# Kernel tuning notes

Hardware: AMD Instinct MI355X
Metric: run time of the kernel (lower is better)

Reference implementation:

```python
import jax, jax.numpy as jnp
import numpy as np

N = 50000      # nodes
E = 800000     # directed edges (avg degree 16 in/out pairs)
F_IN = 16      # dataset.num_features
H = 64         # neuron
S = 7          # Chebyshev order


def setup_inputs() -> dict:
    key = jax.random.key(0)
    ks = jax.random.split(key, 12)
    x = jax.random.normal(ks[0], (N, F_IN), dtype=jnp.float32)
    row = jax.random.randint(ks[1], (E,), 0, N, dtype=jnp.int32)
    off = jax.random.randint(ks[2], (E,), 1, N, dtype=jnp.int32)
    col = (row + off) % N  # guarantees no self-loops (PyG removes them)
    edge_index = jnp.stack([row, col])
    lambda_max = jnp.array([2.0], dtype=jnp.float32)
    def lin(k, fi, fo):
        return jax.random.normal(k, (S, fi, fo), dtype=jnp.float32) * (1.0 / np.sqrt(fi))
    W1 = lin(ks[3], F_IN, H); b1 = jnp.zeros((H,), jnp.float32)
    W2 = lin(ks[4], H, H);    b2 = jnp.zeros((H,), jnp.float32)
    W3 = lin(ks[5], H, H);    b3 = jnp.zeros((H,), jnp.float32)
    Wfc = jax.random.normal(ks[6], (H, 1), dtype=jnp.float32) * (1.0 / np.sqrt(H))
    bfc = jnp.zeros((1,), jnp.float32)
    return {"x": x, "edge_index": edge_index, "lambda_max": lambda_max,
            "W1": W1, "b1": b1, "W2": W2, "b2": b2, "W3": W3, "b3": b3,
            "Wfc": Wfc, "bfc": bfc}


def _make_spmv(edge_index, lam, n):
    # L_hat = 2/lambda_max * (I - D^-1/2 A D^-1/2) - I  (PyG ChebConv sym norm)
    row, col = edge_index[0], edge_index[1]
    deg = jax.ops.segment_sum(jnp.ones_like(row, dtype=jnp.float32), row, num_segments=n)
    dis = jnp.where(deg > 0, jax.lax.rsqrt(jnp.maximum(deg, 1.0)), 0.0)
    w = -(2.0 / lam) * dis[row] * dis[col]      # off-diagonal edge weights
    diag = 2.0 / lam - 1.0                       # self-loop weight
    def spmv(xx):  # L_hat @ xx
        return jax.ops.segment_sum(w[:, None] * xx[col], row, num_segments=n) + diag * xx
    return spmv


def _cheb(xx, W, b, spmv):
    Tx0 = xx
    out = Tx0 @ W[0]
    Tx1 = spmv(Tx0)
    out = out + Tx1 @ W[1]
    for k in range(2, W.shape[0]):  # fixed small S loop
        Tx2 = 2.0 * spmv(Tx1) - Tx0
        out = out + Tx2 @ W[k]
        Tx0, Tx1 = Tx1, Tx2
    return out + b


def reference(x, edge_index, lambda_max, W1, b1, W2, b2, W3, b3, Wfc, bfc):
    lam = lambda_max[0]
    spmv = _make_spmv(edge_index, lam, x.shape[0])
    h = jax.nn.relu(_cheb(x, W1, b1, spmv))
    h = jax.nn.relu(_cheb(h, W2, b2, spmv))
    h = jax.nn.relu(_cheb(h, W3, b3, spmv))
    return h @ Wfc + bfc
```

## Files before the change

### kernel.cpp

```cpp
#include <hip/hip_runtime.h>
#include <math.h>


#define WS_ALIGN(x) (((size_t)(x) + 255) & ~(size_t)255)

using f16x8 = __attribute__((ext_vector_type(8))) _Float16;
using f32x4 = __attribute__((ext_vector_type(4))) float;

__device__ inline float h2f_bits(unsigned int b) {
  unsigned short s = (unsigned short)(b & 0xffffu);
  _Float16 h;
  __builtin_memcpy(&h, &s, 2);
  return (float)h;
}
__device__ inline unsigned short f2h_bits(float f) {
  _Float16 h = (_Float16)f;
  unsigned short s;
  __builtin_memcpy(&s, &h, 2);
  return s;
}
union H8 {
  uint4 q;
  _Float16 h[8];
  ushort us[8];
};

__global__ __launch_bounds__(256) void hist_kernel(const int* __restrict__ row, int E,
                                                   int* __restrict__ deg) {
  int i = blockIdx.x * 256 + threadIdx.x;
  if (i < E) atomicAdd(&deg[row[i]], 1);
}

__global__ __launch_bounds__(256) void scan_sum_kernel(const int* __restrict__ deg,
                                                       int* __restrict__ bsum, int n) {
  int base = blockIdx.x * 1024 + threadIdx.x;
  int v = 0;
#pragma unroll
  for (int u = 0; u < 4; ++u) {
    int i = base + u * 256;
    if (i < n) v += (deg[i] + 7) & ~7;
  }
#pragma unroll
  for (int off = 32; off > 0; off >>= 1) v += __shfl_down(v, off, 64);
  __shared__ int ws[4];
  int lane = threadIdx.x & 63, wave = threadIdx.x >> 6;
  if (lane == 0) ws[wave] = v;
  __syncthreads();
  if (threadIdx.x == 0) bsum[blockIdx.x] = ws[0] + ws[1] + ws[2] + ws[3];
}

__global__ __launch_bounds__(64) void scan_bsum_kernel(int* __restrict__ bsum, int nb) {
  int t = threadIdx.x;
  int v = (t < nb) ? bsum[t] : 0;
  int sc = v;
#pragma unroll
  for (int off = 1; off < 64; off <<= 1) {
    int tv = __shfl_up(sc, off, 64);
    if (t >= off) sc += tv;
  }
  if (t < nb) bsum[t] = sc - v;
}

__global__ __launch_bounds__(256) void scan_out_kernel(const int* __restrict__ deg,
                                                       const int* __restrict__ bsum,
                                                       int* __restrict__ row_ptr,
                                                       int* __restrict__ cursor,
                                                       float* __restrict__ dis, int n) {
  int base = blockIdx.x * 1024 + threadIdx.x * 4;
  int loc[4];
  int s = 0;
#pragma unroll
  for (int u = 0; u < 4; ++u) {
    int i = base + u;
    loc[u] = (i < n) ? deg[i] : 0;
    s += (loc[u] + 7) & ~7;
  }
  int lane = threadIdx.x & 63, wave = threadIdx.x >> 6;
  int sc = s;
#pragma unroll
  for (int off = 1; off < 64; off <<= 1) {
    int tv = __shfl_up(sc, off, 64);
    if (lane >= off) sc += tv;
  }
  __shared__ int wtot[4];
  if (lane == 63) wtot[wave] = sc;
  __syncthreads();
  int pre = sc - s + bsum[blockIdx.x];
  for (int w = 0; w < wave; ++w) pre += wtot[w];
  if (blockIdx.x == 0 && threadIdx.x == 0) row_ptr[0] = 0;
  int running = pre;
#pragma unroll
  for (int u = 0; u < 4; ++u) {
    int i = base + u;
    if (i < n) {
      cursor[i] = running;
      dis[i] = (loc[u] > 0) ? (1.0f / sqrtf((float)loc[u])) : 0.0f;
      running += (loc[u] + 7) & ~7;
      row_ptr[i + 1] = running;
    }
  }
}

__global__ __launch_bounds__(256) void scatter_x8(const int* __restrict__ row,
                                                  const int* __restrict__ col, int E,
                                                  int* __restrict__ cursor,
                                                  const float* __restrict__ dis,
                                                  const float* __restrict__ lamp,
                                                  unsigned int* __restrict__ cw, int n) {
  int c = blockIdx.x & 7;
  int j = blockIdx.x >> 3;
  int nj = gridDim.x >> 3;
  int lo = (c * n) >> 3;
  int hi = ((c + 1) * n) >> 3;
  float sc = -(2.0f / lamp[0]);
  for (int i = j * 256 + threadIdx.x; i < E; i += nj * 256) {
    int r = row[i];
    if (r < lo || r >= hi) continue;
    int cc = col[i];
    int pos = atomicAdd(&cursor[r], 1);
    float w = sc * dis[r] * dis[cc];
    cw[pos] = ((unsigned int)cc << 16) | (unsigned int)f2h_bits(w);
  }
}

__device__ inline void wpk_pack(const float* __restrict__ W, ushort* __restrict__ Wpk,
                                int KREAL, int t) {
  int kt = t >> 8, nt = (t >> 6) & 3, l = t & 63;
  int col = nt * 16 + (l & 15);
  int kb = kt * 32 + ((l >> 4) << 3);
  ushort tmp[8];
#pragma unroll
  for (int j = 0; j < 8; ++j) {
    int k = kb + j;
    float v = (k < KREAL) ? W[(size_t)k * 64 + col] : 0.0f;
    tmp[j] = f2h_bits(v);
  }
  ushort4* dst = (ushort4*)Wpk + (size_t)((kt * 4 + nt) * 64 + l) * 2;
  dst[0] = make_ushort4(tmp[0], tmp[1], tmp[2], tmp[3]);
  dst[1] = make_ushort4(tmp[4], tmp[5], tmp[6], tmp[7]);
}

__global__ __launch_bounds__(256) void prep_all_kernel(
    const float* __restrict__ W1, const float* __restrict__ W2,
    const float* __restrict__ W3, ushort* __restrict__ Wpk1, ushort* __restrict__ Wpk2,
    ushort* __restrict__ Wpk3, const float* __restrict__ x, ushort* __restrict__ T1,
    int n) {
  int b = blockIdx.x;
  if (b < 4) {
    wpk_pack(W1, Wpk1, 112, b * 256 + threadIdx.x);
  } else if (b < 18) {
    wpk_pack(W2, Wpk2, 448, (b - 4) * 256 + threadIdx.x);
  } else if (b < 32) {
    wpk_pack(W3, Wpk3, 448, (b - 18) * 256 + threadIdx.x);
  } else {
    int t = (b - 32) * 256 + threadIdx.x;
    if (t < n * 4) {
      int row = t >> 2, q = t & 3;
      float4 v = ((const float4*)x)[(size_t)row * 4 + q];
      ushort4 o;
      o.x = f2h_bits(v.x);
      o.y = f2h_bits(v.y);
      o.z = f2h_bits(v.z);
      o.w = f2h_bits(v.w);
      ((ushort4*)T1)[(size_t)row * 4 + q] = o;
    } else if (t < n * 8) {
      int t2 = t - n * 4;
      ((ushort4*)(T1 + (size_t)7 * n * 16))[t2] = make_ushort4(0, 0, 0, 0);
    }
  }
}

template <int SW, int MODE, int SLICES>
__global__ __launch_bounds__(256) void spmv_slice(const int* __restrict__ row_ptr,
                                                  const unsigned int* __restrict__ cw,
                                                  const float* __restrict__ lamp,
                                                  const ushort* __restrict__ xin,
                                                  const ushort* __restrict__ sub,
                                                  ushort* __restrict__ xout, int ssz,
                                                  int n) {
  constexpr int LPR = SW / 8;
  constexpr int RPB = 256 / LPR;
  constexpr int B = 8;
  constexpr int EPL = B / LPR;
  int bx = blockIdx.x;
  if (SLICES == 2) {
    int sl = bx & 1;
    bx >>= 1;
    xin += (size_t)sl * ssz;
    if (MODE == 1) sub += (size_t)sl * ssz;
    xout += (size_t)sl * ssz;
  }
  int i = bx * RPB + threadIdx.y;
  if (i >= n) return;
  int f8 = threadIdx.x;
  int lane = (threadIdx.y * LPR + f8) & 63;
  int grpbase = lane - f8;
  float diag = 2.0f / lamp[0] - 1.0f;
  H8 xd;
  xd.q = *(const uint4*)(xin + (size_t)i * SW + f8 * 8);
  float a[8];
#pragma unroll
  for (int j = 0; j < 8; ++j) a[j] = diag * (float)xd.h[j];
  int s = row_ptr[i], e = row_ptr[i + 1];

  for (int j0 = s; j0 < e; j0 += B) {
    unsigned int pv[EPL];
#pragma unroll
    for (int u = 0; u < EPL; ++u) pv[u] = cw[j0 + f8 * EPL + u];
    H8 xv[B];
    float ww[B];
#pragma unroll
    for (int u = 0; u < B; ++u) {
      unsigned int pu = (unsigned int)__shfl((int)pv[u % EPL], grpbase + u / EPL, 64);
      ww[u] = h2f_bits(pu);
      xv[u].q = *(const uint4*)(xin + (size_t)(pu >> 16) * SW + f8 * 8);
    }
#pragma unroll
    for (int u = 0; u < B; ++u)
#pragma unroll
      for (int j = 0; j < 8; ++j) a[j] += ww[u] * (float)xv[u].h[j];
  }

  float r[8];
  if (MODE == 1) {
    H8 sv;
    sv.q = *(const uint4*)(sub + (size_t)i * SW + f8 * 8);
#pragma unroll
    for (int j = 0; j < 8; ++j) r[j] = 2.0f * a[j] - (float)sv.h[j];
  } else {
#pragma unroll
    for (int j = 0; j < 8; ++j) r[j] = a[j];
  }
  H8 o;
#pragma unroll
  for (int j = 0; j < 8; ++j) o.us[j] = f2h_bits(r[j]);
  *(uint4*)(xout + (size_t)i * SW + f8 * 8) = o.q;
}

template <int SW, int KT, bool LAST>
__global__ __launch_bounds__(256) void gemm_mfma(const ushort* __restrict__ A,
                                                 const ushort* __restrict__ Wpk,
                                                 const float* __restrict__ bias,
                                                 ushort* __restrict__ dsth,
                                                 const float* __restrict__ wfc,
                                                 const float* __restrict__ bfc,
                                                 float* __restrict__ dout, int n) {
  int l = threadIdx.x & 63;
  int tile = blockIdx.x * 4 + (threadIdx.x >> 6);
  int r0 = tile * 16;
  if (r0 >= n) return;
  size_t slotsz = (size_t)n * SW;
  int row = r0 + (l & 15);
  const f16x8* bp = (const f16x8*)Wpk + l;
  f32x4 c[4] = {{0.f, 0.f, 0.f, 0.f},
                {0.f, 0.f, 0.f, 0.f},
                {0.f, 0.f, 0.f, 0.f},
                {0.f, 0.f, 0.f, 0.f}};
#pragma unroll
  for (int kt = 0; kt < KT; ++kt) {
    int slot, off;
    if constexpr (SW == 32) {
      slot = kt;
      off = (l >> 4) << 3;
    } else {
      slot = 2 * kt + ((l >> 4) >> 1);
      off = ((l >> 4) & 1) << 3;
    }
    f16x8 af = *(const f16x8*)(A + slot * slotsz + (size_t)row * SW + off);
#pragma unroll
    for (int nt = 0; nt < 4; ++nt) {
      f16x8 bf = bp[(kt * 4 + nt) * 64];
      c[nt] = __builtin_amdgcn_mfma_f32_16x16x32_f16(af, bf, c[nt], 0, 0, 0);
    }
  }
  int rb = r0 + ((l >> 4) << 2);
  int cc = l & 15;
  if (LAST) {
    float bfc0 = bfc[0];
#pragma unroll
    for (int j = 0; j < 4; ++j) {
      float part = 0.0f;
#pragma unroll
      for (int nt = 0; nt < 4; ++nt) {
        int col = nt * 16 + cc;
        part += fmaxf(c[nt][j] + bias[col], 0.0f) * wfc[col];
      }
#pragma unroll
      for (int m = 1; m < 16; m <<= 1) part += __shfl_xor(part, m, 64);
      if (cc == 0) dout[rb + j] = part + bfc0;
    }
  } else {
    size_t dslot = (size_t)n * 32;
#pragma unroll
    for (int nt = 0; nt < 4; ++nt) {
      int col = nt * 16 + cc;
      float bv = bias[col];
      ushort* dbase = dsth + (col >> 5) * dslot + (col & 31);
#pragma unroll
      for (int j = 0; j < 4; ++j) {
        float v = fmaxf(c[nt][j] + bv, 0.0f);
        dbase[(size_t)(rb + j) * 32] = f2h_bits(v);
      }
    }
  }
}

extern "C" void kernel_launch(void* const* d_in, const int* in_sizes, int n_in, void* d_out,
                              int out_size, void* d_ws, size_t ws_size, hipStream_t stream) {
  const float* x = (const float*)d_in[0];
  const int* ei = (const int*)d_in[1];
  const float* lamp = (const float*)d_in[2];
  const float* W1 = (const float*)d_in[3];
  const float* b1 = (const float*)d_in[4];
  const float* W2 = (const float*)d_in[5];
  const float* b2 = (const float*)d_in[6];
  const float* W3 = (const float*)d_in[7];
  const float* b3 = (const float*)d_in[8];
  const float* Wfc = (const float*)d_in[9];
  const float* bfc = (const float*)d_in[10];

  const int N = in_sizes[0] / 16;
  const int E = in_sizes[1] / 2;
  const int* row = ei;
  const int* col = ei + E;

  char* p = (char*)d_ws;
  auto alloc = [&](size_t bytes) {
    char* r = p;
    p += WS_ALIGN(bytes);
    return r;
  };
  const size_t EPAD = (size_t)E + 8 * (size_t)N;
  int* deg = (int*)alloc((size_t)N * 4);
  int* row_ptr = (int*)alloc((size_t)(N + 1) * 4);
  int* cursor = (int*)alloc((size_t)N * 4);
  unsigned int* cw = (unsigned int*)alloc(EPAD * 4);
  float* dis = (float*)alloc((size_t)N * 4);
  int* bsum = (int*)alloc(256 * 4);
  ushort* T1 = (ushort*)alloc((size_t)8 * N * 16 * 2);
  ushort* TXC = (ushort*)alloc((size_t)14 * N * 32 * 2);
  ushort* Wpk1 = (ushort*)alloc((size_t)4 * 256 * 8 * 2);
  ushort* Wpk2 = (ushort*)alloc((size_t)14 * 256 * 8 * 2);
  ushort* Wpk3 = (ushort*)alloc((size_t)14 * 256 * 8 * 2);
  (void)ws_size;
  (void)n_in;
  (void)out_size;

  (void)hipMemsetAsync(deg, 0, (size_t)N * 4, stream);
  (void)hipMemsetAsync(cw, 0, EPAD * 4, stream);
  hist_kernel<<<(E + 255) / 256, 256, 0, stream>>>(row, E, deg);
  int nb = (N + 1023) / 1024;
  scan_sum_kernel<<<nb, 256, 0, stream>>>(deg, bsum, N);
  scan_bsum_kernel<<<1, 64, 0, stream>>>(bsum, nb);
  scan_out_kernel<<<nb, 256, 0, stream>>>(deg, bsum, row_ptr, cursor, dis, N);
  scatter_x8<<<2048, 256, 0, stream>>>(row, col, E, cursor, dis, lamp, cw, N);

  prep_all_kernel<<<32 + (N * 8 + 255) / 256, 256, 0, stream>>>(W1, W2, W3, Wpk1, Wpk2, Wpk3,
                                                                x, T1, N);

  {
    int ssz = N * 16;
    auto S = [&](int k) { return T1 + (size_t)k * ssz; };
    dim3 bs(2, 128);
    int gs = (N + 127) / 128;
    spmv_slice<16, 0, 1><<<gs, bs, 0, stream>>>(row_ptr, cw, lamp, S(0), nullptr, S(1), ssz,
                                                N);
    for (int k = 2; k < 7; ++k)
      spmv_slice<16, 1, 1><<<gs, bs, 0, stream>>>(row_ptr, cw, lamp, S(k - 1), S(k - 2), S(k),
                                                  ssz, N);
    gemm_mfma<16, 4, false><<<(N / 16 + 3) / 4 + 1, 256, 0, stream>>>(T1, Wpk1, b1, TXC,
                                                                      nullptr, nullptr,
                                                                      nullptr, N);
  }

  for (int layer = 2; layer <= 3; ++layer) {
    int ssz = N * 32;
    auto S = [&](int k) { return TXC + (size_t)(2 * k) * ssz; };
    dim3 bs(4, 64);
    int gs = 2 * ((N + 63) / 64);
    spmv_slice<32, 0, 2><<<gs, bs, 0, stream>>>(row_ptr, cw, lamp, S(0), nullptr, S(1), ssz,
                                                N);
    for (int k = 2; k < 7; ++k)
      spmv_slice<32, 1, 2><<<gs, bs, 0, stream>>>(row_ptr, cw, lamp, S(k - 1), S(k - 2), S(k),
                                                  ssz, N);
    if (layer == 2)
      gemm_mfma<32, 14, false><<<(N / 16 + 3) / 4 + 1, 256, 0, stream>>>(TXC, Wpk2, b2, TXC,
                                                                         nullptr, nullptr,
                                                                         nullptr, N);
    else
      gemm_mfma<32, 14, true><<<(N / 16 + 3) / 4 + 1, 256, 0, stream>>>(TXC, Wpk3, b3,
                                                                        nullptr, Wfc, bfc,
                                                                        (float*)d_out, N);
  }
}
```

Measured before the change: 392.0 us.

## Store 64-wide hidden features densely instead of two 32-column slices

Layers 2 and 3 now keep each Chebyshev term as one dense N×64 fp16 array instead of two 32-column slices. Each SpMV launch gathers a full 128-byte row per neighbor using 8 lanes per row, replacing two separate 64-byte slice gathers spread across interleaved blocks. The GEMM addressing and the layer-2 output store are changed to match the new layout. This gives fewer, wider gathers per edge and removes the slice bookkeeping, but it doubles the rows handled per thread group and halves the rows per block, which may change L2 locality across slices.

```diff
diff --git a/kernel.cpp b/kernel.cpp
--- a/kernel.cpp
+++ b/kernel.cpp
@@ -170,27 +170,18 @@
   }
 }
 
-template <int SW, int MODE, int SLICES>
-__global__ __launch_bounds__(256) void spmv_slice(const int* __restrict__ row_ptr,
+template <int SW, int MODE>
+__global__ __launch_bounds__(256) void spmv_dense(const int* __restrict__ row_ptr,
                                                   const unsigned int* __restrict__ cw,
                                                   const float* __restrict__ lamp,
                                                   const ushort* __restrict__ xin,
                                                   const ushort* __restrict__ sub,
-                                                  ushort* __restrict__ xout, int ssz,
-                                                  int n) {
+                                                  ushort* __restrict__ xout, int n) {
   constexpr int LPR = SW / 8;
   constexpr int RPB = 256 / LPR;
   constexpr int B = 8;
   constexpr int EPL = B / LPR;
-  int bx = blockIdx.x;
-  if (SLICES == 2) {
-    int sl = bx & 1;
-    bx >>= 1;
-    xin += (size_t)sl * ssz;
-    if (MODE == 1) sub += (size_t)sl * ssz;
-    xout += (size_t)sl * ssz;
-  }
-  int i = bx * RPB + threadIdx.y;
+  int i = blockIdx.x * RPB + threadIdx.y;
   if (i >= n) return;
   int f8 = threadIdx.x;
   int lane = (threadIdx.y * LPR + f8) & 63;
@@ -259,9 +250,9 @@
 #pragma unroll
   for (int kt = 0; kt < KT; ++kt) {
     int slot, off;
-    if constexpr (SW == 32) {
-      slot = kt;
-      off = (l >> 4) << 3;
+    if constexpr (SW == 64) {
+      slot = kt >> 1;
+      off = ((kt & 1) << 5) + ((l >> 4) << 3);
     } else {
       slot = 2 * kt + ((l >> 4) >> 1);
       off = ((l >> 4) & 1) << 3;
@@ -290,16 +281,14 @@
       if (cc == 0) dout[rb + j] = part + bfc0;
     }
   } else {
-    size_t dslot = (size_t)n * 32;
 #pragma unroll
     for (int nt = 0; nt < 4; ++nt) {
       int col = nt * 16 + cc;
       float bv = bias[col];
-      ushort* dbase = dsth + (col >> 5) * dslot + (col & 31);
 #pragma unroll
       for (int j = 0; j < 4; ++j) {
         float v = fmaxf(c[nt][j] + bv, 0.0f);
-        dbase[(size_t)(rb + j) * 32] = f2h_bits(v);
+        dsth[(size_t)(rb + j) * 64 + col] = f2h_bits(v);
       }
     }
   }
@@ -338,7 +327,7 @@
   float* dis = (float*)alloc((size_t)N * 4);
   int* bsum = (int*)alloc(256 * 4);
   ushort* T1 = (ushort*)alloc((size_t)8 * N * 16 * 2);
-  ushort* TXC = (ushort*)alloc((size_t)14 * N * 32 * 2);
+  ushort* TXC = (ushort*)alloc((size_t)7 * N * 64 * 2);
   ushort* Wpk1 = (ushort*)alloc((size_t)4 * 256 * 8 * 2);
   ushort* Wpk2 = (ushort*)alloc((size_t)14 * 256 * 8 * 2);
   ushort* Wpk3 = (ushort*)alloc((size_t)14 * 256 * 8 * 2);
@@ -363,32 +352,30 @@
     auto S = [&](int k) { return T1 + (size_t)k * ssz; };
     dim3 bs(2, 128);
     int gs = (N + 127) / 128;
-    spmv_slice<16, 0, 1><<<gs, bs, 0, stream>>>(row_ptr, cw, lamp, S(0), nullptr, S(1), ssz,
-                                                N);
+    spmv_dense<16, 0><<<gs, bs, 0, stream>>>(row_ptr, cw, lamp, S(0), nullptr, S(1), N);
     for (int k = 2; k < 7; ++k)
-      spmv_slice<16, 1, 1><<<gs, bs, 0, stream>>>(row_ptr, cw, lamp, S(k - 1), S(k - 2), S(k),
-                                                  ssz, N);
+      spmv_dense<16, 1><<<gs, bs, 0, stream>>>(row_ptr, cw, lamp, S(k - 1), S(k - 2), S(k),
+                                               N);
     gemm_mfma<16, 4, false><<<(N / 16 + 3) / 4 + 1, 256, 0, stream>>>(T1, Wpk1, b1, TXC,
                                                                       nullptr, nullptr,
                                                                       nullptr, N);
   }
 
   for (int layer = 2; layer <= 3; ++layer) {
-    int ssz = N * 32;
-    auto S = [&](int k) { return TXC + (size_t)(2 * k) * ssz; };
-    dim3 bs(4, 64);
-    int gs = 2 * ((N + 63) / 64);
-    spmv_slice<32, 0, 2><<<gs, bs, 0, stream>>>(row_ptr, cw, lamp, S(0), nullptr, S(1), ssz,
-                                                N);
+    int ssz = N * 64;
+    auto S = [&](int k) { return TXC + (size_t)k * ssz; };
+    dim3 bs(8, 32);
+    int gs = (N + 31) / 32;
+    spmv_dense<64, 0><<<gs, bs, 0, stream>>>(row_ptr, cw, lamp, S(0), nullptr, S(1), N);
     for (int k = 2; k < 7; ++k)
-      spmv_slice<32, 1, 2><<<gs, bs, 0, stream>>>(row_ptr, cw, lamp, S(k - 1), S(k - 2), S(k),
-                                                  ssz, N);
+      spmv_dense<64, 1><<<gs, bs, 0, stream>>>(row_ptr, cw, lamp, S(k - 1), S(k - 2), S(k),
+                                               N);
     if (layer == 2)
-      gemm_mfma<32, 14, false><<<(N / 16 + 3) / 4 + 1, 256, 0, stream>>>(TXC, Wpk2, b2, TXC,
+      gemm_mfma<64, 14, false><<<(N / 16 + 3) / 4 + 1, 256, 0, stream>>>(TXC, Wpk2, b2, TXC,
                                                                          nullptr, nullptr,
                                                                          nullptr, N);
     else
-      gemm_mfma<32, 14, true><<<(N / 16 + 3) / 4 + 1, 256, 0, stream>>>(TXC, Wpk3, b3,
+      gemm_mfma<64, 14, true><<<(N / 16 + 3) / 4 + 1, 256, 0, stream>>>(TXC, Wpk3, b3,
                                                                         nullptr, Wfc, bfc,
                                                                         (float*)d_out, N);
   }
```

Result: no change. 389.5 us (median of 2 runs) (-0.6%).

## Fuse six Chebyshev SpMV launches per layer into one cooperative grid-synced kernel

Applied to the files above, without the earlier changes.

Replaces the six separate spmv_slice launches per layer with a single cooperative kernel that loops over Chebyshev orders and uses grid.sync between steps, with a persistent grid sized from occupancy. The goal is to remove per-launch overhead and tail idle time between the dependent SpMV steps. The trade-off is a grid-wide barrier cost per step and a persistent grid capped at 1024 blocks, which may lower the number of gathers in flight compared with full-size launches. The old multi-launch path stays as a fallback if the cooperative launch fails.

```diff
diff --git a/kernel.cpp b/kernel.cpp
--- a/kernel.cpp
+++ b/kernel.cpp
@@ -1,5 +1,8 @@
 #include <hip/hip_runtime.h>
+#include <hip/hip_cooperative_groups.h>
 #include <math.h>
+
+namespace cg = cooperative_groups;
 
 
 #define WS_ALIGN(x) (((size_t)(x) + 255) & ~(size_t)255)
@@ -170,6 +173,83 @@
   }
 }
 
+template <int SW>
+__device__ inline void spmv_row(const int* __restrict__ row_ptr,
+                                const unsigned int* __restrict__ cw, float diag,
+                                const ushort* __restrict__ xin,
+                                const ushort* __restrict__ sub, ushort* __restrict__ xout,
+                                int i, int f8, int grpbase, bool cheb) {
+  constexpr int LPR = SW / 8;
+  constexpr int B = 8;
+  constexpr int EPL = B / LPR;
+  H8 xd;
+  xd.q = *(const uint4*)(xin + (size_t)i * SW + f8 * 8);
+  float a[8];
+#pragma unroll
+  for (int j = 0; j < 8; ++j) a[j] = diag * (float)xd.h[j];
+  int s = row_ptr[i], e = row_ptr[i + 1];
+  for (int j0 = s; j0 < e; j0 += B) {
+    unsigned int pv[EPL];
+#pragma unroll
+    for (int u = 0; u < EPL; ++u) pv[u] = cw[j0 + f8 * EPL + u];
+    H8 xv[B];
+    float ww[B];
+#pragma unroll
+    for (int u = 0; u < B; ++u) {
+      unsigned int pu = (unsigned int)__shfl((int)pv[u % EPL], grpbase + u / EPL, 64);
+      ww[u] = h2f_bits(pu);
+      xv[u].q = *(const uint4*)(xin + (size_t)(pu >> 16) * SW + f8 * 8);
+    }
+#pragma unroll
+    for (int u = 0; u < B; ++u)
+#pragma unroll
+      for (int j = 0; j < 8; ++j) a[j] += ww[u] * (float)xv[u].h[j];
+  }
+  float r[8];
+  if (cheb) {
+    H8 sv;
+    sv.q = *(const uint4*)(sub + (size_t)i * SW + f8 * 8);
+#pragma unroll
+    for (int j = 0; j < 8; ++j) r[j] = 2.0f * a[j] - (float)sv.h[j];
+  } else {
+#pragma unroll
+    for (int j = 0; j < 8; ++j) r[j] = a[j];
+  }
+  H8 o;
+#pragma unroll
+  for (int j = 0; j < 8; ++j) o.us[j] = f2h_bits(r[j]);
+  *(uint4*)(xout + (size_t)i * SW + f8 * 8) = o.q;
+}
+
+template <int SW, int SLICES>
+__global__ __launch_bounds__(256) void coop_cheb(const int* __restrict__ row_ptr,
+                                                 const unsigned int* __restrict__ cw,
+                                                 const float* __restrict__ lamp,
+                                                 ushort* __restrict__ base, int ssz,
+                                                 int n) {
+  constexpr int LPR = SW / 8;
+  constexpr int RPB = 256 / LPR;
+  cg::grid_group grid = cg::this_grid();
+  int sl = (SLICES == 2) ? (blockIdx.x & 1) : 0;
+  int bx = (SLICES == 2) ? (blockIdx.x >> 1) : blockIdx.x;
+  int nbx = (SLICES == 2) ? (gridDim.x >> 1) : gridDim.x;
+  int f8 = threadIdx.x;
+  int ty = threadIdx.y;
+  int lane = (ty * LPR + f8) & 63;
+  int grpbase = lane - f8;
+  float diag = 2.0f / lamp[0] - 1.0f;
+
+  for (int k = 1; k < 7; ++k) {
+    const ushort* xin = base + (size_t)(SLICES * (k - 1) + sl) * ssz;
+    const ushort* sub =
+        (k >= 2) ? (base + (size_t)(SLICES * (k - 2) + sl) * ssz) : (const ushort*)nullptr;
+    ushort* xout = base + (size_t)(SLICES * k + sl) * ssz;
+    for (int i = bx * RPB + ty; i < n; i += nbx * RPB)
+      spmv_row<SW>(row_ptr, cw, diag, xin, sub, xout, i, f8, grpbase, k >= 2);
+    grid.sync();
+  }
+}
+
 template <int SW, int MODE, int SLICES>
 __global__ __launch_bounds__(256) void spmv_slice(const int* __restrict__ row_ptr,
                                                   const unsigned int* __restrict__ cw,
@@ -180,8 +260,6 @@
                                                   int n) {
   constexpr int LPR = SW / 8;
   constexpr int RPB = 256 / LPR;
-  constexpr int B = 8;
-  constexpr int EPL = B / LPR;
   int bx = blockIdx.x;
   if (SLICES == 2) {
     int sl = bx & 1;
@@ -196,45 +274,7 @@
   int lane = (threadIdx.y * LPR + f8) & 63;
   int grpbase = lane - f8;
   float diag = 2.0f / lamp[0] - 1.0f;
-  H8 xd;
-  xd.q = *(const uint4*)(xin + (size_t)i * SW + f8 * 8);
-  float a[8];
-#pragma unroll
-  for (int j = 0; j < 8; ++j) a[j] = diag * (float)xd.h[j];
-  int s = row_ptr[i], e = row_ptr[i + 1];
-
-  for (int j0 = s; j0 < e; j0 += B) {
-    unsigned int pv[EPL];
-#pragma unroll
-    for (int u = 0; u < EPL; ++u) pv[u] = cw[j0 + f8 * EPL + u];
-    H8 xv[B];
-    float ww[B];
-#pragma unroll
-    for (int u = 0; u < B; ++u) {
-      unsigned int pu = (unsigned int)__shfl((int)pv[u % EPL], grpbase + u / EPL, 64);
-      ww[u] = h2f_bits(pu);
-      xv[u].q = *(const uint4*)(xin + (size_t)(pu >> 16) * SW + f8 * 8);
-    }
-#pragma unroll
-    for (int u = 0; u < B; ++u)
-#pragma unroll
-      for (int j = 0; j < 8; ++j) a[j] += ww[u] * (float)xv[u].h[j];
-  }
-
-  float r[8];
-  if (MODE == 1) {
-    H8 sv;
-    sv.q = *(const uint4*)(sub + (size_t)i * SW + f8 * 8);
-#pragma unroll
-    for (int j = 0; j < 8; ++j) r[j] = 2.0f * a[j] - (float)sv.h[j];
-  } else {
-#pragma unroll
-    for (int j = 0; j < 8; ++j) r[j] = a[j];
-  }
-  H8 o;
-#pragma unroll
-  for (int j = 0; j < 8; ++j) o.us[j] = f2h_bits(r[j]);
-  *(uint4*)(xout + (size_t)i * SW + f8 * 8) = o.q;
+  spmv_row<SW>(row_ptr, cw, diag, xin, sub, xout, i, f8, grpbase, MODE == 1);
 }
 
 template <int SW, int KT, bool LAST>
@@ -346,6 +386,24 @@
   (void)n_in;
   (void)out_size;
 
+  int dev = 0;
+  (void)hipGetDevice(&dev);
+  int coopAttr = 0;
+  (void)hipDeviceGetAttribute(&coopAttr, hipDeviceAttributeCooperativeLaunch, dev);
+  int numCU = 0;
+  (void)hipDeviceGetAttribute(&numCU, hipDeviceAttributeMultiprocessorCount, dev);
+  int nb16 = 0, nb32 = 0;
+  (void)hipOccupancyMaxActiveBlocksPerMultiprocessor(&nb16, coop_cheb<16, 1>, 256, 0);
+  (void)hipOccupancyMaxActiveBlocksPerMultiprocessor(&nb32, coop_cheb<32, 2>, 256, 0);
+  int grid16 = numCU * nb16;
+  if (grid16 > 1024) grid16 = 1024;
+  grid16 &= ~7;
+  int grid32 = numCU * nb32;
+  if (grid32 > 1024) grid32 = 1024;
+  grid32 &= ~15;
+  bool coop16 = coopAttr && grid16 >= 64;
+  bool coop32 = coopAttr && grid32 >= 64;
+
   (void)hipMemsetAsync(deg, 0, (size_t)N * 4, stream);
   (void)hipMemsetAsync(cw, 0, EPAD * 4, stream);
   hist_kernel<<<(E + 255) / 256, 256, 0, stream>>>(row, E, deg);
@@ -358,16 +416,27 @@
   prep_all_kernel<<<32 + (N * 8 + 255) / 256, 256, 0, stream>>>(W1, W2, W3, Wpk1, Wpk2, Wpk3,
                                                                 x, T1, N);
 
+  int nI = N;
+
   {
     int ssz = N * 16;
-    auto S = [&](int k) { return T1 + (size_t)k * ssz; };
-    dim3 bs(2, 128);
-    int gs = (N + 127) / 128;
-    spmv_slice<16, 0, 1><<<gs, bs, 0, stream>>>(row_ptr, cw, lamp, S(0), nullptr, S(1), ssz,
-                                                N);
-    for (int k = 2; k < 7; ++k)
-      spmv_slice<16, 1, 1><<<gs, bs, 0, stream>>>(row_ptr, cw, lamp, S(k - 1), S(k - 2), S(k),
-                                                  ssz, N);
+    bool done = false;
+    if (coop16) {
+      void* args[] = {&row_ptr, &cw, &lamp, &T1, &ssz, &nI};
+      hipError_t ce = hipLaunchCooperativeKernel((void*)coop_cheb<16, 1>, dim3(grid16),
+                                                 dim3(2, 128), args, 0, stream);
+      done = (ce == hipSuccess);
+    }
+    if (!done) {
+      auto S = [&](int k) { return T1 + (size_t)k * ssz; };
+      dim3 bs(2, 128);
+      int gs = (N + 127) / 128;
+      spmv_slice<16, 0, 1><<<gs, bs, 0, stream>>>(row_ptr, cw, lamp, S(0), nullptr, S(1), ssz,
+                                                  N);
+      for (int k = 2; k < 7; ++k)
+        spmv_slice<16, 1, 1><<<gs, bs, 0, stream>>>(row_ptr, cw, lamp, S(k - 1), S(k - 2),
+                                                    S(k), ssz, N);
+    }
     gemm_mfma<16, 4, false><<<(N / 16 + 3) / 4 + 1, 256, 0, stream>>>(T1, Wpk1, b1, TXC,
                                                                       nullptr, nullptr,
                                                                       nullptr, N);
@@ -375,14 +444,23 @@
 
   for (int layer = 2; layer <= 3; ++layer) {
     int ssz = N * 32;
-    auto S = [&](int k) { return TXC + (size_t)(2 * k) * ssz; };
-    dim3 bs(4, 64);
-    int gs = 2 * ((N + 63) / 64);
-    spmv_slice<32, 0, 2><<<gs, bs, 0, stream>>>(row_ptr, cw, lamp, S(0), nullptr, S(1), ssz,
-                                                N);
-    for (int k = 2; k < 7; ++k)
-      spmv_slice<32, 1, 2><<<gs, bs, 0, stream>>>(row_ptr, cw, lamp, S(k - 1), S(k - 2), S(k),
-                                                  ssz, N);
+    bool done = false;
+    if (coop32) {
+      void* args[] = {&row_ptr, &cw, &lamp, &TXC, &ssz, &nI};
+      hipError_t ce = hipLaunchCooperativeKernel((void*)coop_cheb<32, 2>, dim3(grid32),
+                                                 dim3(4, 64), args, 0, stream);
+      done = (ce == hipSuccess);
+    }
+    if (!done) {
+      auto S = [&](int k) { return TXC + (size_t)(2 * k) * ssz; };
+      dim3 bs(4, 64);
+      int gs = 2 * ((N + 63) / 64);
+      spmv_slice<32, 0, 2><<<gs, bs, 0, stream>>>(row_ptr, cw, lamp, S(0), nullptr, S(1), ssz,
+                                                  N);
+      for (int k = 2; k < 7; ++k)
+        spmv_slice<32, 1, 2><<<gs, bs, 0, stream>>>(row_ptr, cw, lamp, S(k - 1), S(k - 2),
+                                                    S(k), ssz, N);
+    }
     if (layer == 2)
       gemm_mfma<32, 14, false><<<(N / 16 + 3) / 4 + 1, 256, 0, stream>>>(TXC, Wpk2, b2, TXC,
                                                                          nullptr, nullptr,
```

Result: slower. 1.539 ms (+292.6%).
